# Kernel tuning notes

Measured on AMD Instinct MI355X. Metric: run time of the kernel, lower is better.

Reference implementation:

```python
import jax, jax.numpy as jnp
import numpy as np


def setup_inputs() -> dict:
    key = jax.random.key(0)
    k1, k2, k3 = jax.random.split(key, 3)
    N, M, D = 4096, 4096, 256
    x = jax.random.normal(k1, (N, D), dtype=jnp.float32)
    y = jax.random.normal(k2, (M, D), dtype=jnp.float32)
    # torch init: normal(0.0, 0.1)
    log_band_width = 0.1 * jax.random.normal(k3, (D,), dtype=jnp.float32)
    return {"x": x, "y": y, "log_band_width": log_band_width}


def reference(x, y, log_band_width):
    # ARD kernel: k(x,y) = exp(-0.5 * sum_d (x_d - y_d)^2 / bw_d), bw = exp(log_bw)
    # Quadratic expansion to avoid the O(N*M*D) broadcast intermediate:
    # scale inputs by 1/sqrt(bw), then sqdist = |xw|^2 + |yw|^2 - 2 xw @ yw^T
    inv_sqrt_bw = jnp.exp(-0.5 * log_band_width)  # [D]
    xw = x * inv_sqrt_bw  # [N, D]
    yw = y * inv_sqrt_bw  # [M, D]
    x2 = jnp.sum(xw * xw, axis=-1)  # [N]
    y2 = jnp.sum(yw * yw, axis=-1)  # [M]
    cross = xw @ yw.T  # [N, M] GEMM
    pdist = x2[:, None] + y2[None, :] - 2.0 * cross
    pdist = jnp.maximum(pdist, 0.0)  # clamp tiny negatives from fp cancellation
    return jnp.exp(-0.5 * pdist)
```

## Files before the change

### kernel.cpp

```cpp
#include <hip/hip_runtime.h>
#include <hip/hip_bf16.h>


typedef __attribute__((ext_vector_type(8))) short bf16x8;
typedef __attribute__((ext_vector_type(4))) float f32x4;

#define NN 4096
#define MM 4096
#define DD 256

#define BM 128
#define BN 128
#define BK 32
#define NKT (DD / BK)

#define GLOAD16(gp, lp)                                                        \
    __builtin_amdgcn_global_load_lds(                                          \
        (const __attribute__((address_space(1))) void*)(gp),                   \
        (__attribute__((address_space(3))) void*)(lp), 16, 0, 0)

__global__ __launch_bounds__(256) void ard_prep(
    const float* __restrict__ x, const float* __restrict__ y,
    const float* __restrict__ lbw,
    __hip_bfloat16* __restrict__ xw, __hip_bfloat16* __restrict__ yw,
    float* __restrict__ x2, float* __restrict__ y2)
{
    const int lane = threadIdx.x & 63;
    const int row  = blockIdx.x * 4 + (threadIdx.x >> 6);

    const float* src;
    __hip_bfloat16* dst;
    float* nrm;
    if (row < NN) {
        src = x + (size_t)row * DD;
        dst = xw + (size_t)row * DD;
        nrm = x2 + row;
    } else {
        const int r = row - NN;
        src = y + (size_t)r * DD;
        dst = yw + (size_t)r * DD;
        nrm = y2 + r;
    }

    const float4 v  = reinterpret_cast<const float4*>(src)[lane];
    const float4 lw = reinterpret_cast<const float4*>(lbw)[lane];

    float wv[4];
    wv[0] = v.x * __expf(-0.5f * lw.x);
    wv[1] = v.y * __expf(-0.5f * lw.y);
    wv[2] = v.z * __expf(-0.5f * lw.z);
    wv[3] = v.w * __expf(-0.5f * lw.w);

    __hip_bfloat16 h[4];
    float s = 0.0f;
#pragma unroll
    for (int j = 0; j < 4; ++j) {
        h[j] = __float2bfloat16(wv[j]);
        const float f = __bfloat162float(h[j]);
        s += f * f;
    }

    reinterpret_cast<uint2*>(dst)[lane] = *reinterpret_cast<uint2*>(h);

#pragma unroll
    for (int off = 32; off > 0; off >>= 1) s += __shfl_down(s, off);
    if (lane == 0) *nrm = s;
}

__global__ __launch_bounds__(256) void ard_gemm(
    const __hip_bfloat16* __restrict__ A,
    const __hip_bfloat16* __restrict__ B,
    const float* __restrict__ x2, const float* __restrict__ y2,
    float* __restrict__ out)
{
    __shared__ __align__(16) __hip_bfloat16 sA[2][BM][BK];
    __shared__ __align__(16) __hip_bfloat16 sB[2][BN][BK];

    const int tid  = threadIdx.x;
    const int lane = tid & 63;
    const int wid  = tid >> 6;
    const int wr   = wid >> 1;
    const int wc   = wid & 1;

    const int bi = blockIdx.y;
    const int bj = blockIdx.x;
    const size_t arow0 = (size_t)bi * BM;
    const size_t brow0 = (size_t)bj * BN;

    const int srow = lane >> 2;
    const int scol = (lane & 3) * 8;

    auto stage = [&](int buf, int kt) {
        const int k0 = kt * BK;
        const int rb = wid * 32;
#pragma unroll
        for (int t = 0; t < 2; ++t) {
            const int r = rb + t * 16 + srow;
            GLOAD16(A + (arow0 + r) * DD + k0 + scol, &sA[buf][rb + t * 16][0]);
            GLOAD16(B + (brow0 + r) * DD + k0 + scol, &sB[buf][rb + t * 16][0]);
        }
    };

    f32x4 acc[4][4] = {};

    stage(0, 0);
    __syncthreads();

    const int frow = lane & 15;
    const int fk   = (lane >> 4) * 8;

#pragma unroll
    for (int kt = 0; kt < NKT; ++kt) {
        const int cur = kt & 1;
        if (kt + 1 < NKT) stage(cur ^ 1, kt + 1);

        bf16x8 a[4], b[4];
#pragma unroll
        for (int m = 0; m < 4; ++m)
            a[m] = *reinterpret_cast<const bf16x8*>(&sA[cur][wr * 64 + m * 16 + frow][fk]);
#pragma unroll
        for (int n = 0; n < 4; ++n)
            b[n] = *reinterpret_cast<const bf16x8*>(&sB[cur][wc * 64 + n * 16 + frow][fk]);

#pragma unroll
        for (int m = 0; m < 4; ++m)
#pragma unroll
            for (int n = 0; n < 4; ++n)
                acc[m][n] = __builtin_amdgcn_mfma_f32_16x16x32_bf16(
                    a[m], b[n], acc[m][n], 0, 0, 0);

        __syncthreads();
    }

    const int row0 = bi * BM + wr * 64;
    const int col0 = bj * BN + wc * 64;
    const int cl   = lane & 15;
    const int rsub = (lane >> 4) * 4;

#pragma unroll
    for (int m = 0; m < 4; ++m) {
        const int rbase = row0 + m * 16 + rsub;
        float xv[4];
#pragma unroll
        for (int j = 0; j < 4; ++j) xv[j] = x2[rbase + j];
#pragma unroll
        for (int n = 0; n < 4; ++n) {
            const int c  = col0 + n * 16 + cl;
            const float yv = y2[c];
#pragma unroll
            for (int j = 0; j < 4; ++j) {
                float t = xv[j] + yv - 2.0f * acc[m][n][j];
                t = fmaxf(t, 0.0f);
                out[(size_t)(rbase + j) * MM + c] = __expf(-0.5f * t);
            }
        }
    }
}

extern "C" void kernel_launch(void* const* d_in, const int* in_sizes, int n_in,
                              void* d_out, int out_size, void* d_ws, size_t ws_size,
                              hipStream_t stream) {
    const float* x   = (const float*)d_in[0];
    const float* y   = (const float*)d_in[1];
    const float* lbw = (const float*)d_in[2];
    float* out = (float*)d_out;

    char* ws = (char*)d_ws;
    __hip_bfloat16* xw = (__hip_bfloat16*)ws;
    __hip_bfloat16* yw = (__hip_bfloat16*)(ws + (size_t)2 * 1024 * 1024);
    float* x2 = (float*)(ws + (size_t)4 * 1024 * 1024);
    float* y2 = (float*)(ws + (size_t)4 * 1024 * 1024 + 16384);

    ard_prep<<<(NN + MM) / 4, 256, 0, stream>>>(x, y, lbw, xw, yw, x2, y2);

    dim3 grid(MM / BN, NN / BM);
    ard_gemm<<<grid, 256, 0, stream>>>(xw, yw, x2, y2, out);
}
```

Baseline: 34.76 us.

## Load full K=256 tiles into LDS once with XOR swizzle, drop per-K sync

The GEMM kernel now stages the entire 128x256 A and B tiles (128 KB of LDS total) into shared memory in one pass, replacing the double-buffered BK=32 pipeline. This removes the per-iteration __syncthreads. An XOR swizzle on 16-byte chunks, keyed on row, is applied to the global source addresses and to the fragment reads to avoid LDS bank conflicts. The cost is much higher LDS use per block, so fewer blocks fit per CU. There is also no overlap between global loads and MFMA within a block.

```diff
diff --git a/kernel.cpp b/kernel.cpp
--- a/kernel.cpp
+++ b/kernel.cpp
@@ -11,8 +11,6 @@
 
 #define BM 128
 #define BN 128
-#define BK 32
-#define NKT (DD / BK)
 
 #define GLOAD16(gp, lp)                                                        \
     __builtin_amdgcn_global_load_lds(                                          \
@@ -73,8 +71,8 @@
     const float* __restrict__ x2, const float* __restrict__ y2,
     float* __restrict__ out)
 {
-    __shared__ __align__(16) __hip_bfloat16 sA[2][BM][BK];
-    __shared__ __align__(16) __hip_bfloat16 sB[2][BN][BK];
+    __shared__ __align__(16) __hip_bfloat16 sA[BM * DD];
+    __shared__ __align__(16) __hip_bfloat16 sB[BN * DD];
 
     const int tid  = threadIdx.x;
     const int lane = tid & 63;
@@ -87,49 +85,46 @@
     const size_t arow0 = (size_t)bi * BM;
     const size_t brow0 = (size_t)bj * BN;
 
-    const int srow = lane >> 2;
-    const int scol = (lane & 3) * 8;
+    const int srow = lane >> 5;
+    const int slot = lane & 31;
 
-    auto stage = [&](int buf, int kt) {
-        const int k0 = kt * BK;
-        const int rb = wid * 32;
 #pragma unroll
-        for (int t = 0; t < 2; ++t) {
-            const int r = rb + t * 16 + srow;
-            GLOAD16(A + (arow0 + r) * DD + k0 + scol, &sA[buf][rb + t * 16][0]);
-            GLOAD16(B + (brow0 + r) * DD + k0 + scol, &sB[buf][rb + t * 16][0]);
-        }
-    };
+    for (int t = 0; t < 16; ++t) {
+        const int r    = wid * 32 + t * 2;
+        const int row  = r + srow;
+        const int lcb  = (slot * 16) ^ ((row & 7) << 4);
+        GLOAD16((const char*)(A + (arow0 + row) * DD) + lcb, (char*)sA + r * 512);
+        GLOAD16((const char*)(B + (brow0 + row) * DD) + lcb, (char*)sB + r * 512);
+    }
+    __syncthreads();
 
     f32x4 acc[4][4] = {};
-
-    stage(0, 0);
-    __syncthreads();
-
     const int frow = lane & 15;
-    const int fk   = (lane >> 4) * 8;
+    const int fkb  = (lane >> 4) * 16;
+    const int aswz = (frow & 7) << 4;
 
 #pragma unroll
-    for (int kt = 0; kt < NKT; ++kt) {
-        const int cur = kt & 1;
-        if (kt + 1 < NKT) stage(cur ^ 1, kt + 1);
-
+    for (int kk = 0; kk < 8; ++kk) {
         bf16x8 a[4], b[4];
+        const int kb = kk * 64;
 #pragma unroll
-        for (int m = 0; m < 4; ++m)
-            a[m] = *reinterpret_cast<const bf16x8*>(&sA[cur][wr * 64 + m * 16 + frow][fk]);
+        for (int m = 0; m < 4; ++m) {
+            const int row = wr * 64 + m * 16 + frow;
+            a[m] = *reinterpret_cast<const bf16x8*>(
+                (const char*)sA + row * 512 + ((kb + fkb) ^ aswz));
+        }
 #pragma unroll
-        for (int n = 0; n < 4; ++n)
-            b[n] = *reinterpret_cast<const bf16x8*>(&sB[cur][wc * 64 + n * 16 + frow][fk]);
-
+        for (int n = 0; n < 4; ++n) {
+            const int row = wc * 64 + n * 16 + frow;
+            b[n] = *reinterpret_cast<const bf16x8*>(
+                (const char*)sB + row * 512 + ((kb + fkb) ^ aswz));
+        }
 #pragma unroll
         for (int m = 0; m < 4; ++m)
 #pragma unroll
             for (int n = 0; n < 4; ++n)
                 acc[m][n] = __builtin_amdgcn_mfma_f32_16x16x32_bf16(
                     a[m], b[n], acc[m][n], 0, 0, 0);
-
-        __syncthreads();
     }
 
     const int row0 = bi * BM + wr * 64;
```

Result: faster. 33.43 us (-3.8%).

## Swizzle LDS tiles and transpose MFMA operands for vectorized output stores

Applied to the files above, without the earlier changes.

Applies an XOR swizzle to the 16-byte chunks of each LDS row, in both the global-to-LDS loads and the fragment reads, to cut bank conflicts on the bf16x8 fragment loads. It also swaps the A/B operands of the MFMA so each lane holds four consecutive output columns. The epilogue can then load y2 as a float4 and write float4 stores instead of scalar strided stores. The output write is the dominant memory traffic, so the store change is meant to improve write coalescing.

```diff
diff --git a/kernel.cpp b/kernel.cpp
--- a/kernel.cpp
+++ b/kernel.cpp
@@ -73,8 +73,8 @@
     const float* __restrict__ x2, const float* __restrict__ y2,
     float* __restrict__ out)
 {
-    __shared__ __align__(16) __hip_bfloat16 sA[2][BM][BK];
-    __shared__ __align__(16) __hip_bfloat16 sB[2][BN][BK];
+    __shared__ __align__(16) char sAb[2][BM * BK * 2];
+    __shared__ __align__(16) char sBb[2][BN * BK * 2];
 
     const int tid  = threadIdx.x;
     const int lane = tid & 63;
@@ -87,27 +87,29 @@
     const size_t arow0 = (size_t)bi * BM;
     const size_t brow0 = (size_t)bj * BN;
 
-    const int srow = lane >> 2;
-    const int scol = (lane & 3) * 8;
+    const int crow = lane >> 2;
+    const int slot = lane & 3;
 
     auto stage = [&](int buf, int kt) {
-        const int k0 = kt * BK;
-        const int rb = wid * 32;
+        const int colb = kt * 64;
+        const int lcb  = colb + ((slot * 16) ^ ((crow & 3) << 4));
 #pragma unroll
         for (int t = 0; t < 2; ++t) {
-            const int r = rb + t * 16 + srow;
-            GLOAD16(A + (arow0 + r) * DD + k0 + scol, &sA[buf][rb + t * 16][0]);
-            GLOAD16(B + (brow0 + r) * DD + k0 + scol, &sB[buf][rb + t * 16][0]);
+            const int r   = wid * 32 + t * 16;
+            const int row = r + crow;
+            GLOAD16((const char*)(A + (arow0 + row) * DD) + lcb, sAb[buf] + r * 64);
+            GLOAD16((const char*)(B + (brow0 + row) * DD) + lcb, sBb[buf] + r * 64);
         }
     };
 
     f32x4 acc[4][4] = {};
+    const int frow = lane & 15;
+    const int fkb  = (lane >> 4) * 16;
+    const int swz  = (frow & 3) << 4;
+    const int rdo  = fkb ^ swz;
 
     stage(0, 0);
     __syncthreads();
-
-    const int frow = lane & 15;
-    const int fk   = (lane >> 4) * 8;
 
 #pragma unroll
     for (int kt = 0; kt < NKT; ++kt) {
@@ -116,18 +118,21 @@
 
         bf16x8 a[4], b[4];
 #pragma unroll
-        for (int m = 0; m < 4; ++m)
-            a[m] = *reinterpret_cast<const bf16x8*>(&sA[cur][wr * 64 + m * 16 + frow][fk]);
+        for (int m = 0; m < 4; ++m) {
+            const int row = wr * 64 + m * 16 + frow;
+            a[m] = *reinterpret_cast<const bf16x8*>(sAb[cur] + row * 64 + rdo);
+        }
 #pragma unroll
-        for (int n = 0; n < 4; ++n)
-            b[n] = *reinterpret_cast<const bf16x8*>(&sB[cur][wc * 64 + n * 16 + frow][fk]);
-
+        for (int n = 0; n < 4; ++n) {
+            const int row = wc * 64 + n * 16 + frow;
+            b[n] = *reinterpret_cast<const bf16x8*>(sBb[cur] + row * 64 + rdo);
+        }
 #pragma unroll
         for (int m = 0; m < 4; ++m)
 #pragma unroll
             for (int n = 0; n < 4; ++n)
                 acc[m][n] = __builtin_amdgcn_mfma_f32_16x16x32_bf16(
-                    a[m], b[n], acc[m][n], 0, 0, 0);
+                    b[n], a[m], acc[m][n], 0, 0, 0);
 
         __syncthreads();
     }
@@ -139,20 +144,19 @@
 
 #pragma unroll
     for (int m = 0; m < 4; ++m) {
-        const int rbase = row0 + m * 16 + rsub;
-        float xv[4];
-#pragma unroll
-        for (int j = 0; j < 4; ++j) xv[j] = x2[rbase + j];
+        const int r = row0 + m * 16 + cl;
+        const float xv = x2[r];
+        float* orow = out + (size_t)r * MM;
 #pragma unroll
         for (int n = 0; n < 4; ++n) {
-            const int c  = col0 + n * 16 + cl;
-            const float yv = y2[c];
-#pragma unroll
-            for (int j = 0; j < 4; ++j) {
-                float t = xv[j] + yv - 2.0f * acc[m][n][j];
-                t = fmaxf(t, 0.0f);
-                out[(size_t)(rbase + j) * MM + c] = __expf(-0.5f * t);
-            }
+            const int c = col0 + n * 16 + rsub;
+            const float4 yv = *reinterpret_cast<const float4*>(y2 + c);
+            f32x4 o;
+            o.x = __expf(-0.5f * fmaxf(xv + yv.x - 2.0f * acc[m][n][0], 0.0f));
+            o.y = __expf(-0.5f * fmaxf(xv + yv.y - 2.0f * acc[m][n][1], 0.0f));
+            o.z = __expf(-0.5f * fmaxf(xv + yv.z - 2.0f * acc[m][n][2], 0.0f));
+            o.w = __expf(-0.5f * fmaxf(xv + yv.w - 2.0f * acc[m][n][3], 0.0f));
+            *reinterpret_cast<f32x4*>(orow + c) = o;
         }
     }
 }
```

Result: slower. 37.38 us (+7.5%).

## Replace LDS-tiled GEMM with register-resident A rows and streamed B fragments

Applied to the files above, without the earlier changes.

Drops shared-memory staging: each block keeps a 32-row band of A fully in registers across the whole K=256 and each wave streams B column fragments straight from global memory, double-buffered in registers. The MFMA operands are swapped so results come out as row-major 4-wide vectors, which allows float4 output stores and a float4 y2 load. The aim is to remove LDS traffic and __syncthreads and to make the output stores wider, since the output write dominates. The cost is reloading B from global/L2 for every 32-row band and heavier register use, which may limit occupancy.

```diff
diff --git a/kernel.cpp b/kernel.cpp
--- a/kernel.cpp
+++ b/kernel.cpp
@@ -9,15 +9,7 @@
 #define MM 4096
 #define DD 256
 
-#define BM 128
-#define BN 128
-#define BK 32
-#define NKT (DD / BK)
-
-#define GLOAD16(gp, lp)                                                        \
-    __builtin_amdgcn_global_load_lds(                                          \
-        (const __attribute__((address_space(1))) void*)(gp),                   \
-        (__attribute__((address_space(3))) void*)(lp), 16, 0, 0)
+#define MFMA_BF16 __builtin_amdgcn_mfma_f32_16x16x32_bf16
 
 __global__ __launch_bounds__(256) void ard_prep(
     const float* __restrict__ x, const float* __restrict__ y,
@@ -73,87 +65,75 @@
     const float* __restrict__ x2, const float* __restrict__ y2,
     float* __restrict__ out)
 {
-    __shared__ __align__(16) __hip_bfloat16 sA[2][BM][BK];
-    __shared__ __align__(16) __hip_bfloat16 sB[2][BN][BK];
-
     const int tid  = threadIdx.x;
     const int lane = tid & 63;
     const int wid  = tid >> 6;
-    const int wr   = wid >> 1;
-    const int wc   = wid & 1;
 
-    const int bi = blockIdx.y;
-    const int bj = blockIdx.x;
-    const size_t arow0 = (size_t)bi * BM;
-    const size_t brow0 = (size_t)bj * BN;
+    const int bid   = blockIdx.x;
+    const int band  = bid >> 3;
+    const int q     = bid & 7;
+    const int row0  = band * 32;
+    const int wcol0 = q * 512 + wid * 128;
 
-    const int srow = lane >> 2;
-    const int scol = (lane & 3) * 8;
+    const int cl = lane & 15;
+    const int g  = lane >> 4;
 
-    auto stage = [&](int buf, int kt) {
-        const int k0 = kt * BK;
-        const int rb = wid * 32;
+    bf16x8 afr[2][8];
 #pragma unroll
-        for (int t = 0; t < 2; ++t) {
-            const int r = rb + t * 16 + srow;
-            GLOAD16(A + (arow0 + r) * DD + k0 + scol, &sA[buf][rb + t * 16][0]);
-            GLOAD16(B + (brow0 + r) * DD + k0 + scol, &sB[buf][rb + t * 16][0]);
-        }
+    for (int m = 0; m < 2; ++m) {
+        const char* ap = (const char*)(A + (size_t)(row0 + m * 16 + cl) * DD) + g * 16;
+#pragma unroll
+        for (int kt = 0; kt < 8; ++kt)
+            afr[m][kt] = *reinterpret_cast<const bf16x8*>(ap + kt * 64);
+    }
+
+    const float xv0 = x2[row0 + cl];
+    const float xv1 = x2[row0 + 16 + cl];
+    float* const orow0 = out + (size_t)(row0 + cl) * MM;
+    float* const orow1 = out + (size_t)(row0 + 16 + cl) * MM;
+
+    auto loadB = [&](bf16x8* bf, int cf) {
+        const char* bp = (const char*)(B + (size_t)(wcol0 + cf * 16 + cl) * DD) + g * 16;
+#pragma unroll
+        for (int kt = 0; kt < 8; ++kt)
+            bf[kt] = *reinterpret_cast<const bf16x8*>(bp + kt * 64);
     };
 
-    f32x4 acc[4][4] = {};
+    auto compute = [&](const bf16x8* bf, int cf) {
+        f32x4 p0 = {}, p1 = {}, p2 = {}, p3 = {};
+#pragma unroll
+        for (int kt = 0; kt < 8; kt += 2) {
+            p0 = MFMA_BF16(bf[kt],     afr[0][kt],     p0, 0, 0, 0);
+            p1 = MFMA_BF16(bf[kt + 1], afr[0][kt + 1], p1, 0, 0, 0);
+            p2 = MFMA_BF16(bf[kt],     afr[1][kt],     p2, 0, 0, 0);
+            p3 = MFMA_BF16(bf[kt + 1], afr[1][kt + 1], p3, 0, 0, 0);
+        }
+        const f32x4 acc0 = p0 + p1;
+        const f32x4 acc1 = p2 + p3;
 
-    stage(0, 0);
-    __syncthreads();
+        const int c = wcol0 + cf * 16 + g * 4;
+        const float4 yv = *reinterpret_cast<const float4*>(y2 + c);
+        f32x4 o;
+        o.x = __expf(-0.5f * fmaxf(xv0 + yv.x - 2.0f * acc0[0], 0.0f));
+        o.y = __expf(-0.5f * fmaxf(xv0 + yv.y - 2.0f * acc0[1], 0.0f));
+        o.z = __expf(-0.5f * fmaxf(xv0 + yv.z - 2.0f * acc0[2], 0.0f));
+        o.w = __expf(-0.5f * fmaxf(xv0 + yv.w - 2.0f * acc0[3], 0.0f));
+        *reinterpret_cast<f32x4*>(orow0 + c) = o;
+        o.x = __expf(-0.5f * fmaxf(xv1 + yv.x - 2.0f * acc1[0], 0.0f));
+        o.y = __expf(-0.5f * fmaxf(xv1 + yv.y - 2.0f * acc1[1], 0.0f));
+        o.z = __expf(-0.5f * fmaxf(xv1 + yv.z - 2.0f * acc1[2], 0.0f));
+        o.w = __expf(-0.5f * fmaxf(xv1 + yv.w - 2.0f * acc1[3], 0.0f));
+        *reinterpret_cast<f32x4*>(orow1 + c) = o;
+    };
 
-    const int frow = lane & 15;
-    const int fk   = (lane >> 4) * 8;
-
+    bf16x8 bb0[8], bb1[8];
+    loadB(bb0, 0);
 #pragma unroll
-    for (int kt = 0; kt < NKT; ++kt) {
-        const int cur = kt & 1;
-        if (kt + 1 < NKT) stage(cur ^ 1, kt + 1);
-
-        bf16x8 a[4], b[4];
-#pragma unroll
-        for (int m = 0; m < 4; ++m)
-            a[m] = *reinterpret_cast<const bf16x8*>(&sA[cur][wr * 64 + m * 16 + frow][fk]);
-#pragma unroll
-        for (int n = 0; n < 4; ++n)
-            b[n] = *reinterpret_cast<const bf16x8*>(&sB[cur][wc * 64 + n * 16 + frow][fk]);
-
-#pragma unroll
-        for (int m = 0; m < 4; ++m)
-#pragma unroll
-            for (int n = 0; n < 4; ++n)
-                acc[m][n] = __builtin_amdgcn_mfma_f32_16x16x32_bf16(
-                    a[m], b[n], acc[m][n], 0, 0, 0);
-
-        __syncthreads();
-    }
-
-    const int row0 = bi * BM + wr * 64;
-    const int col0 = bj * BN + wc * 64;
-    const int cl   = lane & 15;
-    const int rsub = (lane >> 4) * 4;
-
-#pragma unroll
-    for (int m = 0; m < 4; ++m) {
-        const int rbase = row0 + m * 16 + rsub;
-        float xv[4];
-#pragma unroll
-        for (int j = 0; j < 4; ++j) xv[j] = x2[rbase + j];
-#pragma unroll
-        for (int n = 0; n < 4; ++n) {
-            const int c  = col0 + n * 16 + cl;
-            const float yv = y2[c];
-#pragma unroll
-            for (int j = 0; j < 4; ++j) {
-                float t = xv[j] + yv - 2.0f * acc[m][n][j];
-                t = fmaxf(t, 0.0f);
-                out[(size_t)(rbase + j) * MM + c] = __expf(-0.5f * t);
-            }
-        }
+    for (int p = 0; p < 4; ++p) {
+        loadB(bb1, 2 * p + 1);
+        compute(bb0, 2 * p);
+        if (p < 3) loadB(bb0, 2 * p + 2);
+        compute(bb1, 2 * p + 1);
     }
 }
 
@@ -173,6 +153,5 @@
 
     ard_prep<<<(NN + MM) / 4, 256, 0, stream>>>(x, y, lbw, xw, yw, x2, y2);
 
-    dim3 grid(MM / BN, NN / BM);
-    ard_gemm<<<grid, 256, 0, stream>>>(xw, yw, x2, y2, out);
+    ard_gemm<<<1024, 256, 0, stream>>>(xw, yw, x2, y2, out);
 }
```

Result: slower. 52.16 us (+50.1%).
